# Performance work log

Hardware: AMD Instinct MI355X
Metric: run time of the kernel (lower is better)

Reference implementation:

```python
import jax, jax.numpy as jnp
import numpy as np

N_NODES = 50000
N_EDGES = 800000
IN_CH = 384
HID = 128


def _gcn_conv(x, src, dst, W, b, n):
    # PyG GCNConv: h = x @ W; out[dst] += d^-1/2[src] * d^-1/2[dst] * h[src]; out += b
    h = x @ W  # [N, out_ch]
    deg = jax.ops.segment_sum(jnp.ones(src.shape, dtype=h.dtype), dst, num_segments=n)
    dinv = jnp.where(deg > 0, jax.lax.rsqrt(jnp.maximum(deg, 1.0)), 0.0)
    norm = dinv[src] * dinv[dst]  # [E]
    out = jax.ops.segment_sum(h[src] * norm[:, None], dst, num_segments=n)
    return out + b


def setup_inputs() -> dict:
    key = jax.random.key(0)
    k_x, k_e, k1, k2, k3, k4 = jax.random.split(key, 6)
    x = jax.random.normal(k_x, (N_NODES, IN_CH), dtype=jnp.float32)
    edge_index = jax.random.randint(k_e, (2, N_EDGES), 0, N_NODES, dtype=jnp.int64)
    s1 = 1.0 / np.sqrt(IN_CH)
    s2 = 1.0 / np.sqrt(HID)
    W1 = jax.random.uniform(k1, (IN_CH, HID), jnp.float32, -s1, s1)
    b1 = jnp.zeros((HID,), jnp.float32)
    W2 = jax.random.uniform(k2, (HID, HID), jnp.float32, -s2, s2)
    b2 = jnp.zeros((HID,), jnp.float32)
    return {"x": x, "edge_index": edge_index, "W1": W1, "b1": b1, "W2": W2, "b2": b2}


def reference(x, edge_index, W1, b1, W2, b2):
    n = x.shape[0]
    loops = jnp.arange(n, dtype=edge_index.dtype)
    src = jnp.concatenate([edge_index[0], loops])  # add_self_loops
    dst = jnp.concatenate([edge_index[1], loops])
    h = _gcn_conv(x, src, dst, W1, b1, n)
    h = jax.nn.relu(h)  # dropout is identity in eval mode
    out = _gcn_conv(h, src, dst, W2, b2, n)
    return out
```

## Files before the change

kernel.cpp:

```cpp
#include <hip/hip_runtime.h>
#include <hip/hip_fp16.h>

#define NN 50000
#define NE 800000
#define C_IN 384
#define C_HID 128
#define NB 196
#define CHK 128
#define ECH 6250
#define NBKT 128
#define BSTR 392

typedef __attribute__((ext_vector_type(8))) short short8;
typedef __attribute__((ext_vector_type(4))) float f32x4;
typedef __attribute__((ext_vector_type(4))) unsigned short us4;

__device__ __forceinline__ ushort f2bf(float x) {
    uint u = __float_as_uint(x);
    uint r = (u + 0x7fffu + ((u >> 16) & 1u)) >> 16;
    return (ushort)r;
}
__device__ __forceinline__ float bf2f(ushort b) { return __uint_as_float(((uint)b) << 16); }

__global__ __launch_bounds__(256) void k_dinv(const int* __restrict__ cnt,
                                              float* __restrict__ dinv) {
    int i = blockIdx.x * 256 + threadIdx.x;
    if (i < NN) dinv[i] = rsqrtf((float)cnt[i] + 1.0f);
}

__global__ __launch_bounds__(256) void k_bsum(const int* __restrict__ cnt,
                                              int* __restrict__ bsum) {
    __shared__ int part[256];
    const int tid = threadIdx.x;
    const int i = blockIdx.x * 256 + tid;
    part[tid] = (i < NN) ? cnt[i] : 0;
    __syncthreads();
#pragma unroll
    for (int off = 128; off > 0; off >>= 1) {
        if (tid < off) part[tid] += part[tid + off];
        __syncthreads();
    }
    if (tid == 0) bsum[blockIdx.x] = part[0];
}

__global__ __launch_bounds__(256) void k_sbs(const int* __restrict__ bsum,
                                             int* __restrict__ bpre) {
    __shared__ int part[256];
    const int t = threadIdx.x;
    part[t] = (t < NB) ? bsum[t] : 0;
    __syncthreads();
#pragma unroll
    for (int off = 1; off < 256; off <<= 1) {
        int v = (t >= off) ? part[t - off] : 0;
        __syncthreads();
        part[t] += v;
        __syncthreads();
    }
    if (t < NB) bpre[t] = (t == 0) ? 0 : part[t - 1];
}

__global__ __launch_bounds__(256) void k_write(const int* __restrict__ cnt,
                                               const int* __restrict__ bpre,
                                               int* __restrict__ rowptr) {
    __shared__ int part[256];
    const int t = threadIdx.x;
    const int i = blockIdx.x * 256 + t;
    const int v = (i < NN) ? cnt[i] : 0;
    part[t] = v;
    __syncthreads();
#pragma unroll
    for (int off = 1; off < 256; off <<= 1) {
        int u = (t >= off) ? part[t - off] : 0;
        __syncthreads();
        part[t] += u;
        __syncthreads();
    }
    if (i < NN) {
        const int excl = bpre[blockIdx.x] + part[t] - v;
        rowptr[i] = excl;
        if (i == NN - 1) rowptr[NN] = excl + v;
    }
}

__global__ __launch_bounds__(256) void k_hist(const int* __restrict__ dst,
                                              int* __restrict__ histT) {
    __shared__ int h[NBKT];
    const int tid = threadIdx.x;
    if (tid < NBKT) h[tid] = 0;
    __syncthreads();
    const int base = blockIdx.x * ECH;
    for (int i = base + tid; i < base + ECH; i += 256)
        atomicAdd(&h[(uint)dst[i] / BSTR], 1);
    __syncthreads();
    if (tid < NBKT) histT[tid * CHK + blockIdx.x] = h[tid];
}

__global__ __launch_bounds__(1024) void k_hscan(const int* __restrict__ histT,
                                                int* __restrict__ histS) {
    __shared__ int part[1024];
    const int t = threadIdx.x;
    const int base = t * 16;
    int loc[16];
    int s = 0;
#pragma unroll
    for (int i = 0; i < 16; ++i) {
        loc[i] = histT[base + i];
        s += loc[i];
    }
    part[t] = s;
    __syncthreads();
    for (int off = 1; off < 1024; off <<= 1) {
        int v = (t >= off) ? part[t - off] : 0;
        __syncthreads();
        part[t] += v;
        __syncthreads();
    }
    int run = (t == 0) ? 0 : part[t - 1];
#pragma unroll
    for (int i = 0; i < 16; ++i) {
        histS[base + i] = run;
        run += loc[i];
    }
}

__global__ __launch_bounds__(256) void k_binscat(const int* __restrict__ src,
                                                 const int* __restrict__ dst,
                                                 const int* __restrict__ histS,
                                                 uint2* __restrict__ mid) {
    __shared__ int cur[NBKT];
    const int tid = threadIdx.x;
    if (tid < NBKT) cur[tid] = histS[tid * CHK + blockIdx.x];
    __syncthreads();
    const int base = blockIdx.x * ECH;
    for (int i = base + tid; i < base + ECH; i += 256) {
        const int s = src[i];
        const int d = dst[i];
        const int p = atomicAdd(&cur[(uint)d / BSTR], 1);
        mid[p] = make_uint2((uint)d, (uint)s << 16);
    }
}

__global__ __launch_bounds__(256) void k_bcnt(const uint2* __restrict__ mid,
                                              const int* __restrict__ histS,
                                              int* __restrict__ cnt) {
    __shared__ int cur[BSTR];
    const int tid = threadIdx.x;
    const int b = blockIdx.x;
    for (int j = tid; j < BSTR; j += 256) cur[j] = 0;
    __syncthreads();
    const int lo = histS[b * CHK];
    const int hi = (b < NBKT - 1) ? histS[(b + 1) * CHK] : NE;
    for (int e = lo + tid; e < hi; e += 256)
        atomicAdd(&cur[mid[e].x - (uint)b * BSTR], 1);
    __syncthreads();
    for (int j = tid; j < BSTR; j += 256) {
        const int idx = b * BSTR + j;
        if (idx < NN) cnt[idx] = cur[j];
    }
}

__global__ __launch_bounds__(256) void k_binfill(const uint2* __restrict__ mid,
                                                 const int* __restrict__ histS,
                                                 const int* __restrict__ rowptr,
                                                 const float* __restrict__ dinv,
                                                 uint* __restrict__ csr) {
    __shared__ int cur[BSTR];
    __shared__ float sdv[BSTR];
    const int tid = threadIdx.x;
    const int b = blockIdx.x;
    for (int j = tid; j < BSTR; j += 256) {
        const int idx = b * BSTR + j;
        cur[j] = (idx < NN) ? rowptr[idx] : 0;
        sdv[j] = (idx < NN) ? dinv[idx] : 0.f;
    }
    __syncthreads();
    const int lo = histS[b * CHK];
    const int hi = (b < NBKT - 1) ? histS[(b + 1) * CHK] : NE;
    for (int e = lo + tid; e < hi; e += 256) {
        const uint2 u = mid[e];
        const int j = u.x - (uint)b * BSTR;
        const float norm = dinv[u.y >> 16] * sdv[j];
        const int p = atomicAdd(&cur[j], 1);
        csr[p] = u.y | __half_as_ushort(__float2half(norm));
    }
}

__global__ __launch_bounds__(256) void k_wconv(const float* __restrict__ W,
                                               ushort* __restrict__ Wt,
                                               int K) {
    int i = blockIdx.x * 256 + threadIdx.x;
    if (i < K * C_HID) {
        int k = i >> 7, n = i & 127;
        float w = W[i];
        ushort h = f2bf(w);
        ushort l = f2bf(w - bf2f(h));
        int blk = k >> 6, khalf = (k >> 5) & 1, kq = (k >> 3) & 3, j = k & 7;
        int t = n >> 4, fr = n & 15, lane = kq * 16 + fr;
        size_t off = (size_t)blk * 16384 + (size_t)((khalf * 8 + t) * 64 + lane) * 8 + j;
        Wt[off] = h;
        Wt[off + 8192] = l;
    }
}

template <bool IN_RELU_BIAS, bool OUT_BIAS>
__global__ __launch_bounds__(256) void k_gemm_mfma(const float* __restrict__ X,
                                                   const ushort* __restrict__ Wt,
                                                   const float* __restrict__ bin,
                                                   const float* __restrict__ bout,
                                                   const float* __restrict__ dinv,
                                                   ushort* __restrict__ out_main,
                                                   float* __restrict__ out_self,
                                                   int K) {
    __shared__ short8 Bs8[2048];

    const int tid = threadIdx.x;
    const int bm = blockIdx.x * 32;
    const int wv = tid >> 6;
    const int lane = tid & 63;
    const int fr = lane & 15;
    const int kq = lane >> 4;
    const int g = wv >> 1;
    const int ch = wv & 1;

    int row = bm + g * 16 + fr;
    if (row >= NN) row = NN - 1;
    const float* xrow = X + (size_t)row * K + kq * 8;
    const short8* Wt8 = (const short8*)Wt;

    f32x4 acc[4];
#pragma unroll
    for (int t = 0; t < 4; ++t) acc[t] = (f32x4){0.f, 0.f, 0.f, 0.f};

    float4 xa0 = *(const float4*)(xrow);
    float4 xa1 = *(const float4*)(xrow + 4);
    float4 xb0 = *(const float4*)(xrow + 32);
    float4 xb1 = *(const float4*)(xrow + 36);
    short8 tmp[8];
#pragma unroll
    for (int i = 0; i < 8; ++i) tmp[i] = Wt8[i * 256 + tid];

    for (int k0 = 0; k0 < K; k0 += 64) {
        float xv[16] = {xa0.x, xa0.y, xa0.z, xa0.w, xa1.x, xa1.y, xa1.z, xa1.w,
                        xb0.x, xb0.y, xb0.z, xb0.w, xb1.x, xb1.y, xb1.z, xb1.w};
        if (IN_RELU_BIAS) {
            const float* bp = bin + k0 + kq * 8;
            float4 b0 = *(const float4*)(bp);
            float4 b1 = *(const float4*)(bp + 4);
            float4 b2 = *(const float4*)(bp + 32);
            float4 b3 = *(const float4*)(bp + 36);
            const float bb[16] = {b0.x, b0.y, b0.z, b0.w, b1.x, b1.y, b1.z, b1.w,
                                  b2.x, b2.y, b2.z, b2.w, b3.x, b3.y, b3.z, b3.w};
#pragma unroll
            for (int j = 0; j < 16; ++j) xv[j] = fmaxf(xv[j] + bb[j], 0.f);
        }
        union { ushort u[8]; short8 v; } ah0, al0, ah1, al1;
#pragma unroll
        for (int j = 0; j < 8; ++j) {
            uint u = __float_as_uint(xv[j]);
            ah0.u[j] = (ushort)(u >> 16);
            al0.u[j] = (ushort)(__float_as_uint(xv[j] - __uint_as_float(u & 0xffff0000u)) >> 16);
            uint w = __float_as_uint(xv[8 + j]);
            ah1.u[j] = (ushort)(w >> 16);
            al1.u[j] = (ushort)(__float_as_uint(xv[8 + j] - __uint_as_float(w & 0xffff0000u)) >> 16);
        }

        __syncthreads();
#pragma unroll
        for (int i = 0; i < 8; ++i) Bs8[i * 256 + tid] = tmp[i];
        __syncthreads();

        if (k0 + 64 < K) {
            const float* ap = xrow + k0 + 64;
            xa0 = *(const float4*)(ap);
            xa1 = *(const float4*)(ap + 4);
            xb0 = *(const float4*)(ap + 32);
            xb1 = *(const float4*)(ap + 36);
            const short8* gB = Wt8 + (size_t)((k0 >> 6) + 1) * 2048;
#pragma unroll
            for (int i = 0; i < 8; ++i) tmp[i] = gB[i * 256 + tid];
        }

#pragma unroll
        for (int t = 0; t < 4; ++t) {
            const int tt = ch * 4 + t;
            const short8 bh0 = Bs8[tt * 64 + lane];
            const short8 bl0 = Bs8[1024 + tt * 64 + lane];
            const short8 bh1 = Bs8[(8 + tt) * 64 + lane];
            const short8 bl1 = Bs8[1024 + (8 + tt) * 64 + lane];
            acc[t] = __builtin_amdgcn_mfma_f32_16x16x32_bf16(ah0.v, bh0, acc[t], 0, 0, 0);
            acc[t] = __builtin_amdgcn_mfma_f32_16x16x32_bf16(ah0.v, bl0, acc[t], 0, 0, 0);
            acc[t] = __builtin_amdgcn_mfma_f32_16x16x32_bf16(al0.v, bh0, acc[t], 0, 0, 0);
            acc[t] = __builtin_amdgcn_mfma_f32_16x16x32_bf16(ah1.v, bh1, acc[t], 0, 0, 0);
            acc[t] = __builtin_amdgcn_mfma_f32_16x16x32_bf16(ah1.v, bl1, acc[t], 0, 0, 0);
            acc[t] = __builtin_amdgcn_mfma_f32_16x16x32_bf16(al1.v, bh1, acc[t], 0, 0, 0);
        }
    }

#pragma unroll
    for (int r = 0; r < 4; ++r) {
        const int m = bm + g * 16 + kq * 4 + r;
        if (m < NN) {
            const float dv = dinv[m];
            const float d2 = dv * dv;
            ushort* om = out_main + (size_t)m * C_HID;
            float* os = out_self + (size_t)m * C_HID;
#pragma unroll
            for (int t = 0; t < 4; ++t) {
                const int n = (ch * 4 + t) * 16 + fr;
                const float v = acc[t][r];
                om[n] = f2bf(v);
                os[n] = v * d2 + (OUT_BIAS ? bout[n] : 0.f);
            }
        }
    }
}

__global__ __launch_bounds__(256) void k_gather(const ushort* __restrict__ h,
                                                const int* __restrict__ rowptr,
                                                const uint* __restrict__ csr,
                                                float* __restrict__ out) {
    const int tid = threadIdx.x;
    const int node = blockIdx.x * 8 + (tid >> 5);
    if (node >= NN) return;
    const int lane = tid & 31;
    const int c = lane * 4;
    const int beg = rowptr[node];
    const int end = rowptr[node + 1];

    float4 acc = *(const float4*)(out + (size_t)node * C_HID + c);

    for (int j0 = beg; j0 < end; j0 += 32) {
        const int n = end - j0;
        uint myE = 0;
        if (lane < n) myE = csr[j0 + lane];
        const int m = n < 32 ? n : 32;
        int jj = 0;
        for (; jj + 4 <= m; jj += 4) {
            const uint e0 = (uint)__shfl((int)myE, jj + 0, 32);
            const uint e1 = (uint)__shfl((int)myE, jj + 1, 32);
            const uint e2 = (uint)__shfl((int)myE, jj + 2, 32);
            const uint e3 = (uint)__shfl((int)myE, jj + 3, 32);
            const us4 u0 = *(const us4*)(h + (size_t)(e0 >> 16) * C_HID + c);
            const us4 u1 = *(const us4*)(h + (size_t)(e1 >> 16) * C_HID + c);
            const us4 u2 = *(const us4*)(h + (size_t)(e2 >> 16) * C_HID + c);
            const us4 u3 = *(const us4*)(h + (size_t)(e3 >> 16) * C_HID + c);
            const float n0 = __half2float(__ushort_as_half((ushort)(e0 & 0xffffu)));
            const float n1 = __half2float(__ushort_as_half((ushort)(e1 & 0xffffu)));
            const float n2 = __half2float(__ushort_as_half((ushort)(e2 & 0xffffu)));
            const float n3 = __half2float(__ushort_as_half((ushort)(e3 & 0xffffu)));
            acc.x = fmaf(bf2f(u0[0]), n0, acc.x);
            acc.y = fmaf(bf2f(u0[1]), n0, acc.y);
            acc.z = fmaf(bf2f(u0[2]), n0, acc.z);
            acc.w = fmaf(bf2f(u0[3]), n0, acc.w);
            acc.x = fmaf(bf2f(u1[0]), n1, acc.x);
            acc.y = fmaf(bf2f(u1[1]), n1, acc.y);
            acc.z = fmaf(bf2f(u1[2]), n1, acc.z);
            acc.w = fmaf(bf2f(u1[3]), n1, acc.w);
            acc.x = fmaf(bf2f(u2[0]), n2, acc.x);
            acc.y = fmaf(bf2f(u2[1]), n2, acc.y);
            acc.z = fmaf(bf2f(u2[2]), n2, acc.z);
            acc.w = fmaf(bf2f(u2[3]), n2, acc.w);
            acc.x = fmaf(bf2f(u3[0]), n3, acc.x);
            acc.y = fmaf(bf2f(u3[1]), n3, acc.y);
            acc.z = fmaf(bf2f(u3[2]), n3, acc.z);
            acc.w = fmaf(bf2f(u3[3]), n3, acc.w);
        }
        for (; jj < m; ++jj) {
            const uint ev = (uint)__shfl((int)myE, jj, 32);
            const us4 u = *(const us4*)(h + (size_t)(ev >> 16) * C_HID + c);
            const float nw = __half2float(__ushort_as_half((ushort)(ev & 0xffffu)));
            acc.x = fmaf(bf2f(u[0]), nw, acc.x);
            acc.y = fmaf(bf2f(u[1]), nw, acc.y);
            acc.z = fmaf(bf2f(u[2]), nw, acc.z);
            acc.w = fmaf(bf2f(u[3]), nw, acc.w);
        }
    }
    *(float4*)(out + (size_t)node * C_HID + c) = acc;
}

extern "C" void kernel_launch(void* const* d_in, const int* in_sizes, int n_in,
                              void* d_out, int out_size, void* d_ws, size_t ws_size,
                              hipStream_t stream) {
    const float* x = (const float*)d_in[0];
    const int* ei = (const int*)d_in[1];
    const float* W1 = (const float*)d_in[2];
    const float* b1 = (const float*)d_in[3];
    const float* W2 = (const float*)d_in[4];
    const float* b2 = (const float*)d_in[5];
    float* out = (float*)d_out;

    const int* src = ei;
    const int* dst = ei + NE;

    int* cnt = (int*)d_ws;
    int* rowptr = cnt + 50048;
    float* dinv = (float*)(rowptr + 50064);
    int* bsum = (int*)(dinv + 50048);
    int* bpre = bsum + 256;
    int* histT = bpre + 256;
    int* histS = histT + 16384;
    ushort* Wt1 = (ushort*)(histS + 16384);
    ushort* Wt2 = Wt1 + 98304;
    uint* csr = (uint*)(Wt2 + 32768);
    uint2* mid = (uint2*)(csr + NE);
    ushort* A_bf = (ushort*)(mid + NE);
    float* B = (float*)(A_bf + (size_t)NN * C_HID);

    k_wconv<<<(C_IN * C_HID + 255) / 256, 256, 0, stream>>>(W1, Wt1, C_IN);
    k_wconv<<<(C_HID * C_HID + 255) / 256, 256, 0, stream>>>(W2, Wt2, C_HID);
    k_hist<<<CHK, 256, 0, stream>>>(dst, histT);
    k_hscan<<<1, 1024, 0, stream>>>(histT, histS);
    k_binscat<<<CHK, 256, 0, stream>>>(src, dst, histS, mid);
    k_bcnt<<<NBKT, 256, 0, stream>>>(mid, histS, cnt);
    k_dinv<<<NB, 256, 0, stream>>>(cnt, dinv);
    k_bsum<<<NB, 256, 0, stream>>>(cnt, bsum);
    k_sbs<<<1, 256, 0, stream>>>(bsum, bpre);
    k_write<<<NB, 256, 0, stream>>>(cnt, bpre, rowptr);
    k_binfill<<<NBKT, 256, 0, stream>>>(mid, histS, rowptr, dinv, csr);

    const int gblocks = (NN + 31) / 32;
    const int agblocks = (NN + 7) / 8;
    k_gemm_mfma<false, false><<<gblocks, 256, 0, stream>>>(x, Wt1, nullptr, nullptr, dinv, A_bf, B, C_IN);
    k_gather<<<agblocks, 256, 0, stream>>>(A_bf, rowptr, csr, B);
    k_gemm_mfma<true, true><<<gblocks, 256, 0, stream>>>(B, Wt2, b1, b2, dinv, A_bf, out, C_HID);
    k_gather<<<agblocks, 256, 0, stream>>>(A_bf, rowptr, csr, out);
}
```

Before: 319.1 us.

## Load GEMM weight fragments directly from global memory, drop LDS staging

The MFMA GEMM kernel no longer stages the pre-swizzled weight tile through shared memory with two block barriers per K step. Each wave now loads its own B fragments straight from global (L2/L1-cached) memory into registers, and launch bounds request four blocks per CU. This removes LDS traffic and barriers and frees shared memory for occupancy, but it gives up the register prefetch of the next weight tile. Weight loads may now stall the MFMAs and are duplicated across the two row-group waves.

Result: slower. 354.7 us (+11.1%).

```diff
diff --git a/kernel.cpp b/kernel.cpp
--- a/kernel.cpp
+++ b/kernel.cpp
@@ -203,16 +203,14 @@
 }
 
 template <bool IN_RELU_BIAS, bool OUT_BIAS>
-__global__ __launch_bounds__(256) void k_gemm_mfma(const float* __restrict__ X,
-                                                   const ushort* __restrict__ Wt,
-                                                   const float* __restrict__ bin,
-                                                   const float* __restrict__ bout,
-                                                   const float* __restrict__ dinv,
-                                                   ushort* __restrict__ out_main,
-                                                   float* __restrict__ out_self,
-                                                   int K) {
-    __shared__ short8 Bs8[2048];
-
+__global__ __launch_bounds__(256, 4) void k_gemm_mfma(const float* __restrict__ X,
+                                                      const ushort* __restrict__ Wt,
+                                                      const float* __restrict__ bin,
+                                                      const float* __restrict__ bout,
+                                                      const float* __restrict__ dinv,
+                                                      ushort* __restrict__ out_main,
+                                                      float* __restrict__ out_self,
+                                                      int K) {
     const int tid = threadIdx.x;
     const int bm = blockIdx.x * 32;
     const int wv = tid >> 6;
@@ -235,11 +233,19 @@
     float4 xa1 = *(const float4*)(xrow + 4);
     float4 xb0 = *(const float4*)(xrow + 32);
     float4 xb1 = *(const float4*)(xrow + 36);
-    short8 tmp[8];
-#pragma unroll
-    for (int i = 0; i < 8; ++i) tmp[i] = Wt8[i * 256 + tid];
 
     for (int k0 = 0; k0 < K; k0 += 64) {
+        const short8* gB = Wt8 + (size_t)(k0 >> 6) * 2048;
+        short8 b_h0[4], b_l0[4], b_h1[4], b_l1[4];
+#pragma unroll
+        for (int t = 0; t < 4; ++t) {
+            const int tt = ch * 4 + t;
+            b_h0[t] = gB[tt * 64 + lane];
+            b_l0[t] = gB[1024 + tt * 64 + lane];
+            b_h1[t] = gB[(8 + tt) * 64 + lane];
+            b_l1[t] = gB[1024 + (8 + tt) * 64 + lane];
+        }
+
         float xv[16] = {xa0.x, xa0.y, xa0.z, xa0.w, xa1.x, xa1.y, xa1.z, xa1.w,
                         xb0.x, xb0.y, xb0.z, xb0.w, xb1.x, xb1.y, xb1.z, xb1.w};
         if (IN_RELU_BIAS) {
@@ -264,35 +270,22 @@
             al1.u[j] = (ushort)(__float_as_uint(xv[8 + j] - __uint_as_float(w & 0xffff0000u)) >> 16);
         }
 
-        __syncthreads();
-#pragma unroll
-        for (int i = 0; i < 8; ++i) Bs8[i * 256 + tid] = tmp[i];
-        __syncthreads();
-
         if (k0 + 64 < K) {
             const float* ap = xrow + k0 + 64;
             xa0 = *(const float4*)(ap);
             xa1 = *(const float4*)(ap + 4);
             xb0 = *(const float4*)(ap + 32);
             xb1 = *(const float4*)(ap + 36);
-            const short8* gB = Wt8 + (size_t)((k0 >> 6) + 1) * 2048;
-#pragma unroll
-            for (int i = 0; i < 8; ++i) tmp[i] = gB[i * 256 + tid];
         }
 
 #pragma unroll
         for (int t = 0; t < 4; ++t) {
-            const int tt = ch * 4 + t;
-            const short8 bh0 = Bs8[tt * 64 + lane];
-            const short8 bl0 = Bs8[1024 + tt * 64 + lane];
-            const short8 bh1 = Bs8[(8 + tt) * 64 + lane];
-            const short8 bl1 = Bs8[1024 + (8 + tt) * 64 + lane];
-            acc[t] = __builtin_amdgcn_mfma_f32_16x16x32_bf16(ah0.v, bh0, acc[t], 0, 0, 0);
-            acc[t] = __builtin_amdgcn_mfma_f32_16x16x32_bf16(ah0.v, bl0, acc[t], 0, 0, 0);
-            acc[t] = __builtin_amdgcn_mfma_f32_16x16x32_bf16(al0.v, bh0, acc[t], 0, 0, 0);
-            acc[t] = __builtin_amdgcn_mfma_f32_16x16x32_bf16(ah1.v, bh1, acc[t], 0, 0, 0);
-            acc[t] = __builtin_amdgcn_mfma_f32_16x16x32_bf16(ah1.v, bl1, acc[t], 0, 0, 0);
-            acc[t] = __builtin_amdgcn_mfma_f32_16x16x32_bf16(al1.v, bh1, acc[t], 0, 0, 0);
+            acc[t] = __builtin_amdgcn_mfma_f32_16x16x32_bf16(ah0.v, b_h0[t], acc[t], 0, 0, 0);
+            acc[t] = __builtin_amdgcn_mfma_f32_16x16x32_bf16(ah0.v, b_l0[t], acc[t], 0, 0, 0);
+            acc[t] = __builtin_amdgcn_mfma_f32_16x16x32_bf16(al0.v, b_h0[t], acc[t], 0, 0, 0);
+            acc[t] = __builtin_amdgcn_mfma_f32_16x16x32_bf16(ah1.v, b_h1[t], acc[t], 0, 0, 0);
+            acc[t] = __builtin_amdgcn_mfma_f32_16x16x32_bf16(ah1.v, b_l1[t], acc[t], 0, 0, 0);
+            acc[t] = __builtin_amdgcn_mfma_f32_16x16x32_bf16(al1.v, b_h1[t], acc[t], 0, 0, 0);
         }
     }
 
```

## Double-buffer weight tiles in LDS with a single barrier per k-step

Applied to the files above, without the earlier changes.

Splits the shared weight tile into two ping-pong buffers so the next tile is written while the current one is consumed, replacing two __syncthreads per iteration with one raw barrier. The activation prefetch is deepened to two k-steps using two register sets and a manually unrolled loop. This targets global-load and barrier stalls in the two-layer dense GEMM, at the cost of twice the LDS (64KB) and more registers, which may reduce occupancy. The loop assumes the number of k-blocks is even (384/64 and 128/64 both are).

Measured after the change: 316.1 us. About the same (-1.0%).

```diff
diff --git a/kernel.cpp b/kernel.cpp
--- a/kernel.cpp
+++ b/kernel.cpp
@@ -211,7 +211,7 @@
                                                    ushort* __restrict__ out_main,
                                                    float* __restrict__ out_self,
                                                    int K) {
-    __shared__ short8 Bs8[2048];
+    __shared__ short8 Bs8[2][2048];
 
     const int tid = threadIdx.x;
     const int bm = blockIdx.x * 32;
@@ -226,30 +226,46 @@
     if (row >= NN) row = NN - 1;
     const float* xrow = X + (size_t)row * K + kq * 8;
     const short8* Wt8 = (const short8*)Wt;
+    const int NK = K >> 6;
 
     f32x4 acc[4];
 #pragma unroll
     for (int t = 0; t < 4; ++t) acc[t] = (f32x4){0.f, 0.f, 0.f, 0.f};
 
-    float4 xa0 = *(const float4*)(xrow);
-    float4 xa1 = *(const float4*)(xrow + 4);
-    float4 xb0 = *(const float4*)(xrow + 32);
-    float4 xb1 = *(const float4*)(xrow + 36);
     short8 tmp[8];
 #pragma unroll
     for (int i = 0; i < 8; ++i) tmp[i] = Wt8[i * 256 + tid];
-
-    for (int k0 = 0; k0 < K; k0 += 64) {
-        float xv[16] = {xa0.x, xa0.y, xa0.z, xa0.w, xa1.x, xa1.y, xa1.z, xa1.w,
-                        xb0.x, xb0.y, xb0.z, xb0.w, xb1.x, xb1.y, xb1.z, xb1.w};
+    float4 a00 = *(const float4*)(xrow);
+    float4 a01 = *(const float4*)(xrow + 4);
+    float4 a02 = *(const float4*)(xrow + 32);
+    float4 a03 = *(const float4*)(xrow + 36);
+    const float* ap1 = xrow + 64;
+    float4 a10 = *(const float4*)(ap1);
+    float4 a11 = *(const float4*)(ap1 + 4);
+    float4 a12 = *(const float4*)(ap1 + 32);
+    float4 a13 = *(const float4*)(ap1 + 36);
+#pragma unroll
+    for (int i = 0; i < 8; ++i) Bs8[0][i * 256 + tid] = tmp[i];
+    asm volatile("s_waitcnt lgkmcnt(0)" ::: "memory");
+    __builtin_amdgcn_s_barrier();
+
+    auto ITER = [&](int kb, float4& A0, float4& A1, float4& A2, float4& A3) {
+        const bool nxt = (kb + 1 < NK);
+        if (nxt) {
+            const short8* gW = Wt8 + (size_t)(kb + 1) * 2048;
+#pragma unroll
+            for (int i = 0; i < 8; ++i) tmp[i] = gW[i * 256 + tid];
+        }
+        float xv[16] = {A0.x, A0.y, A0.z, A0.w, A1.x, A1.y, A1.z, A1.w,
+                        A2.x, A2.y, A2.z, A2.w, A3.x, A3.y, A3.z, A3.w};
         if (IN_RELU_BIAS) {
-            const float* bp = bin + k0 + kq * 8;
-            float4 b0 = *(const float4*)(bp);
-            float4 b1 = *(const float4*)(bp + 4);
-            float4 b2 = *(const float4*)(bp + 32);
-            float4 b3 = *(const float4*)(bp + 36);
-            const float bb[16] = {b0.x, b0.y, b0.z, b0.w, b1.x, b1.y, b1.z, b1.w,
-                                  b2.x, b2.y, b2.z, b2.w, b3.x, b3.y, b3.z, b3.w};
+            const float* bp = bin + kb * 64 + kq * 8;
+            float4 c0 = *(const float4*)(bp);
+            float4 c1 = *(const float4*)(bp + 4);
+            float4 c2 = *(const float4*)(bp + 32);
+            float4 c3 = *(const float4*)(bp + 36);
+            const float bb[16] = {c0.x, c0.y, c0.z, c0.w, c1.x, c1.y, c1.z, c1.w,
+                                  c2.x, c2.y, c2.z, c2.w, c3.x, c3.y, c3.z, c3.w};
 #pragma unroll
             for (int j = 0; j < 16; ++j) xv[j] = fmaxf(xv[j] + bb[j], 0.f);
         }
@@ -263,30 +279,21 @@
             ah1.u[j] = (ushort)(w >> 16);
             al1.u[j] = (ushort)(__float_as_uint(xv[8 + j] - __uint_as_float(w & 0xffff0000u)) >> 16);
         }
-
-        __syncthreads();
-#pragma unroll
-        for (int i = 0; i < 8; ++i) Bs8[i * 256 + tid] = tmp[i];
-        __syncthreads();
-
-        if (k0 + 64 < K) {
-            const float* ap = xrow + k0 + 64;
-            xa0 = *(const float4*)(ap);
-            xa1 = *(const float4*)(ap + 4);
-            xb0 = *(const float4*)(ap + 32);
-            xb1 = *(const float4*)(ap + 36);
-            const short8* gB = Wt8 + (size_t)((k0 >> 6) + 1) * 2048;
-#pragma unroll
-            for (int i = 0; i < 8; ++i) tmp[i] = gB[i * 256 + tid];
-        }
-
+        if (kb + 2 < NK) {
+            const float* ap = xrow + (kb + 2) * 64;
+            A0 = *(const float4*)(ap);
+            A1 = *(const float4*)(ap + 4);
+            A2 = *(const float4*)(ap + 32);
+            A3 = *(const float4*)(ap + 36);
+        }
+        const short8* bs = Bs8[kb & 1];
 #pragma unroll
         for (int t = 0; t < 4; ++t) {
             const int tt = ch * 4 + t;
-            const short8 bh0 = Bs8[tt * 64 + lane];
-            const short8 bl0 = Bs8[1024 + tt * 64 + lane];
-            const short8 bh1 = Bs8[(8 + tt) * 64 + lane];
-            const short8 bl1 = Bs8[1024 + (8 + tt) * 64 + lane];
+            const short8 bh0 = bs[tt * 64 + lane];
+            const short8 bl0 = bs[1024 + tt * 64 + lane];
+            const short8 bh1 = bs[(8 + tt) * 64 + lane];
+            const short8 bl1 = bs[1024 + (8 + tt) * 64 + lane];
             acc[t] = __builtin_amdgcn_mfma_f32_16x16x32_bf16(ah0.v, bh0, acc[t], 0, 0, 0);
             acc[t] = __builtin_amdgcn_mfma_f32_16x16x32_bf16(ah0.v, bl0, acc[t], 0, 0, 0);
             acc[t] = __builtin_amdgcn_mfma_f32_16x16x32_bf16(al0.v, bh0, acc[t], 0, 0, 0);
@@ -294,6 +301,17 @@
             acc[t] = __builtin_amdgcn_mfma_f32_16x16x32_bf16(ah1.v, bl1, acc[t], 0, 0, 0);
             acc[t] = __builtin_amdgcn_mfma_f32_16x16x32_bf16(al1.v, bh1, acc[t], 0, 0, 0);
         }
+        if (nxt) {
+#pragma unroll
+            for (int i = 0; i < 8; ++i) Bs8[(kb + 1) & 1][i * 256 + tid] = tmp[i];
+            asm volatile("s_waitcnt lgkmcnt(0)" ::: "memory");
+            __builtin_amdgcn_s_barrier();
+        }
+    };
+
+    for (int kb = 0; kb < NK; kb += 2) {
+        ITER(kb, a00, a01, a02, a03);
+        ITER(kb + 1, a10, a11, a12, a13);
     }
 
 #pragma unroll
```
